# Optimization experiments

Measured on AMD Instinct MI355X. Metric: run time of the kernel, lower is better.

## Reference

```python
import jax, jax.numpy as jnp
import numpy as np

S, B, IN_DIM, HID, NT, TAPELEN = 256, 64, 128, 128, 2, 128
DIM = HID // NT          # per-tape cell width
LH = HID // 2            # LSTM hidden per direction


def _uniform(k, shape, fan):
    bound = 1.0 / np.sqrt(fan)
    return jax.random.uniform(k, shape, jnp.float32, -bound, bound)


def setup_inputs() -> dict:
    key = jax.random.key(0)
    ks = jax.random.split(key, 17)
    return {
        "inputs": jax.random.normal(ks[0], (S, B, IN_DIM), jnp.float32),
        "tapelen": TAPELEN,
        # bidirectional LSTM (torch gate order i,f,g,o)
        "W_ih_f": _uniform(ks[1], (4 * LH, IN_DIM), LH),
        "W_hh_f": _uniform(ks[2], (4 * LH, LH), LH),
        "b_ih_f": _uniform(ks[3], (4 * LH,), LH),
        "b_hh_f": _uniform(ks[4], (4 * LH,), LH),
        "W_ih_r": _uniform(ks[5], (4 * LH, IN_DIM), LH),
        "W_hh_r": _uniform(ks[6], (4 * LH, LH), LH),
        "b_ih_r": _uniform(ks[7], (4 * LH,), LH),
        "b_hh_r": _uniform(ks[8], (4 * LH,), LH),
        "W_act": _uniform(ks[9], (8 * NT, HID), HID),
        "b_act": _uniform(ks[10], (8 * NT,), HID),
        "W_val": _uniform(ks[11], (DIM * NT, IN_DIM), IN_DIM),
        "b_val": _uniform(ks[12], (DIM * NT,), IN_DIM),
        "W_out": _uniform(ks[13], (HID, HID), HID),
        "b_out": _uniform(ks[14], (HID,), HID),
    }


def _lstm_dir(x, Wih, Whh, bih, bhh, reverse):
    Hh = Whh.shape[1]
    bsz = x.shape[1]
    bias = bih + bhh

    def step(carry, xt):
        h, c = carry
        g = xt @ Wih.T + h @ Whh.T + bias
        i, f, gg, o = jnp.split(g, 4, axis=-1)
        c = jax.nn.sigmoid(f) * c + jax.nn.sigmoid(i) * jnp.tanh(gg)
        h = jax.nn.sigmoid(o) * jnp.tanh(c)
        return (h, c), h

    init = (jnp.zeros((bsz, Hh), x.dtype), jnp.zeros((bsz, Hh), x.dtype))
    _, hs = jax.lax.scan(step, init, x, reverse=reverse)
    return hs


def _nam_forward(inputs, tapelen, W_ih_f, W_hh_f, b_ih_f, b_hh_f,
                 W_ih_r, W_hh_r, b_ih_r, b_hh_r,
                 W_act, b_act, W_val, b_val, W_out, b_out):
    seqlen, bsz, _ = inputs.shape
    n_tapes = W_act.shape[0] // 8
    dim = W_val.shape[0] // n_tapes

    values = (inputs @ W_val.T + b_val).reshape(seqlen, bsz, n_tapes, dim)

    h_fwd = _lstm_dir(inputs, W_ih_f, W_hh_f, b_ih_f, b_hh_f, reverse=False)
    h_rev = _lstm_dir(inputs, W_ih_r, W_hh_r, b_ih_r, b_hh_r, reverse=True)
    hidden_control = jnp.concatenate([h_fwd, h_rev], axis=-1)  # [S,B,HID]

    actions = (hidden_control @ W_act.T + b_act).reshape(seqlen, bsz, n_tapes, 8)
    dir_r = jax.nn.softmax(actions[..., :3], axis=-1)
    dir_w = jax.nn.softmax(actions[..., 3:6], axis=-1)
    rwprobs = jax.nn.sigmoid(actions[..., 6:])

    tape0 = jnp.zeros((tapelen, bsz, n_tapes, dim), inputs.dtype)
    pos0 = jnp.zeros((tapelen, bsz, n_tapes), inputs.dtype).at[0].set(1.0)

    def step(carry, xs):
        tape, rpos, wpos = carry
        val, rdir, wdir, rw = xs  # [B,T,C], [B,T,3], [B,T,3], [B,T,2]
        oldval = jnp.einsum('lntc,lnt->ntc', tape, wpos)
        newmem = jnp.einsum('lnt,ntc->lntc', wpos, val - oldval)
        tape = tape + newmem * rw[None, :, :, 1:2]
        # NOTE: faithful to original — write-position shift uses rolls of rpos
        next_w = jnp.roll(rpos, 1, axis=0)
        prev_w = jnp.roll(rpos, -1, axis=0)
        wpos = (prev_w * wdir[None, :, :, 0] + wpos * wdir[None, :, :, 1]
                + next_w * wdir[None, :, :, 2])
        read_out = jnp.einsum('lntc,lnt->ntc', tape, rpos * rw[None, :, :, 0])
        next_r = jnp.roll(rpos, 1, axis=0)
        prev_r = jnp.roll(rpos, -1, axis=0)
        rpos = (prev_r * rdir[None, :, :, 0] + rpos * rdir[None, :, :, 1]
                + next_r * rdir[None, :, :, 2])
        return (tape, rpos, wpos), read_out

    (tape, rpos, wpos), read_outs = jax.lax.scan(
        step, (tape0, pos0, pos0), (values, dir_r, dir_w, rwprobs))

    outputs = read_outs.reshape(seqlen, bsz, -1) @ W_out.T + b_out
    return outputs, tape, rpos, wpos


def reference(inputs, tapelen, W_ih_f, W_hh_f, b_ih_f, b_hh_f,
              W_ih_r, W_hh_r, b_ih_r, b_hh_r,
              W_act, b_act, W_val, b_val, W_out, b_out):
    return _nam_forward(inputs, tapelen, W_ih_f, W_hh_f, b_ih_f, b_hh_f,
                        W_ih_r, W_hh_r, b_ih_r, b_hh_r,
                        W_act, b_act, W_val, b_val, W_out, b_out)
```

## Files before the change

### kernel.cpp

```cpp
#include <hip/hip_runtime.h>


typedef unsigned short u16;
typedef __attribute__((ext_vector_type(8))) __bf16 bf16x8;
typedef __attribute__((ext_vector_type(4))) float f32x4;

__device__ __forceinline__ u16 f2bf(float x) {
  unsigned u = __builtin_bit_cast(unsigned, x);
  u += 0x7fffu + ((u >> 16) & 1u);
  return (u16)(u >> 16);
}
__device__ __forceinline__ float sigm_f(float x) { return 1.f / (1.f + __expf(-x)); }
__device__ __forceinline__ float tanh_f(float x) { return 1.f - 2.f / (__expf(2.f * x) + 1.f); }

struct ConvArgs {
  const float* src[8];
  u16* dst[8];
  int off[9];
};

__global__ __launch_bounds__(256) void k_convert(ConvArgs a) {
  int total = a.off[8];
  for (int i = blockIdx.x * 256 + threadIdx.x; i < total; i += gridDim.x * 256) {
    int s = 0;
#pragma unroll
    for (int k = 1; k < 8; ++k) s += (i >= a.off[k]);
    int j = i - a.off[s];
    a.dst[s][j] = f2bf(a.src[s][j]);
  }
}

__device__ __forceinline__ void gemm_tile(const u16* A, const u16* W,
                                          const float* b1, const float* b2,
                                          float* C, int mt, int nt, int N, int lane) {
  const int rc = lane & 15;
  const int kq = lane >> 4;
  f32x4 acc = {0.f, 0.f, 0.f, 0.f};
#pragma unroll
  for (int kc = 0; kc < 4; ++kc) {
    bf16x8 av = *(const bf16x8*)(A + (size_t)(mt * 16 + rc) * 128 + kc * 32 + kq * 8);
    bf16x8 wv = *(const bf16x8*)(W + (size_t)(nt * 16 + rc) * 128 + kc * 32 + kq * 8);
    acc = __builtin_amdgcn_mfma_f32_16x16x32_bf16(av, wv, acc, 0, 0, 0);
  }
  const int n = nt * 16 + rc;
  float bias = b1[n] + (b2 ? b2[n] : 0.f);
  const int m0 = mt * 16 + kq * 4;
#pragma unroll
  for (int j = 0; j < 4; ++j) C[(size_t)(m0 + j) * N + n] = acc[j] + bias;
}

__global__ __launch_bounds__(256) void k_gemm_in(
    const u16* Abf, const u16* Wf, const u16* Wr, const u16* Wv,
    const float* bihf, const float* bhhf, const float* bihr, const float* bhhr,
    const float* bval, float* xf, float* xr, float* val) {
  int lane = threadIdx.x & 63;
  int wid = blockIdx.x * 4 + (threadIdx.x >> 6);
  if (wid < 16384) {
    gemm_tile(Abf, Wf, bihf, bhhf, xf, wid >> 4, wid & 15, 256, lane);
  } else if (wid < 32768) {
    int w2 = wid - 16384;
    gemm_tile(Abf, Wr, bihr, bhhr, xr, w2 >> 4, w2 & 15, 256, lane);
  } else {
    int w2 = wid - 32768;
    gemm_tile(Abf, Wv, bval, nullptr, val, w2 >> 3, w2 & 7, 128, lane);
  }
}

__global__ __launch_bounds__(256) void k_gemm_act(const u16* A, const u16* W,
                                                  const float* b1, float* C) {
  int lane = threadIdx.x & 63;
  int wid = blockIdx.x * 4 + (threadIdx.x >> 6);
  gemm_tile(A, W, b1, nullptr, C, wid, 0, 16, lane);
}

__global__ __launch_bounds__(256) void k_gemm_out(const u16* A, const u16* W,
                                                  const float* b1, float* C) {
  int lane = threadIdx.x & 63;
  int wid = blockIdx.x * 4 + (threadIdx.x >> 6);
  gemm_tile(A, W, b1, nullptr, C, wid >> 3, wid & 7, 128, lane);
}

__global__ __launch_bounds__(256) void k_lstm(
    const u16* Whhf, const u16* Whhr, const float* xpf, const float* xpr,
    u16* hidden_bf ) {
  const int tid = threadIdx.x;
  const int lane = tid & 63;
  const int v = __builtin_amdgcn_readfirstlane(tid >> 6);
  const int dir = blockIdx.x & 1;
  const int b_base = (blockIdx.x >> 1) * 16;
  const u16* Whh = dir ? Whhr : Whhf;
  const float* xp = dir ? xpr : xpf;

  __shared__ u16 h_lds[2][1024];
  for (int i = tid; i < 1024; i += 256) h_lds[0][i] = 0;

  const int cl = lane & 15;
  const int kq = lane >> 4;
  const int nbase = v * 16 + cl;
  const int rbase = b_base + kq * 4;

  bf16x8 wf[4][2];
#pragma unroll
  for (int gt = 0; gt < 4; ++gt)
#pragma unroll
    for (int kc = 0; kc < 2; ++kc)
      wf[gt][kc] = *(const bf16x8*)(Whh + (size_t)(gt * 64 + nbase) * 64 + kc * 32 + kq * 8);

  float c4[4] = {0.f, 0.f, 0.f, 0.f};
  float x0[16], x1[16];

#define LOADX(dst, ss)                                                       \
  _Pragma("unroll") for (int gt = 0; gt < 4; ++gt)                           \
  _Pragma("unroll") for (int j = 0; j < 4; ++j)                              \
    dst[gt * 4 + j] = xp[((size_t)(ss)*64 + rbase + j) * 256 + gt * 64 + nbase];

  { int s0 = dir ? 255 : 0; LOADX(x0, s0); }
  { int s1 = dir ? 254 : 1; LOADX(x1, s1); }

#define LSTM_STEP(XB, IT)                                                     \
  {                                                                           \
    const int it_ = (IT);                                                     \
    const int s_ = dir ? (255 - it_) : it_;                                   \
    __syncthreads();                                                          \
    bf16x8 af[2];                                                             \
    _Pragma("unroll") for (int kc = 0; kc < 2; ++kc) {                        \
      unsigned off = ((unsigned)(cl * 128 + kc * 64 + kq * 16)) ^             \
                     ((unsigned)(cl & 7) << 4);                               \
      af[kc] = *(const bf16x8*)((const char*)h_lds[it_ & 1] + off);           \
    }                                                                         \
    f32x4 acc[4];                                                             \
    _Pragma("unroll") for (int gt = 0; gt < 4; ++gt) {                        \
      f32x4 t_;                                                               \
      t_[0] = XB[gt * 4 + 0]; t_[1] = XB[gt * 4 + 1];                         \
      t_[2] = XB[gt * 4 + 2]; t_[3] = XB[gt * 4 + 3];                         \
      acc[gt] = t_;                                                           \
    }                                                                         \
    if (it_ + 2 < 256) { int sp_ = dir ? (253 - it_) : (it_ + 2); LOADX(XB, sp_); } \
    _Pragma("unroll") for (int kc = 0; kc < 2; ++kc)                          \
    _Pragma("unroll") for (int gt = 0; gt < 4; ++gt)                          \
      acc[gt] = __builtin_amdgcn_mfma_f32_16x16x32_bf16(af[kc], wf[gt][kc],   \
                                                        acc[gt], 0, 0, 0);    \
    u16* hw = h_lds[(it_ + 1) & 1];                                           \
    _Pragma("unroll") for (int j = 0; j < 4; ++j) {                           \
      float gi = sigm_f(acc[0][j]);                                           \
      float gf = sigm_f(acc[1][j]);                                           \
      float gg = tanh_f(acc[2][j]);                                           \
      float go = sigm_f(acc[3][j]);                                           \
      float cc = gf * c4[j] + gi * gg;                                        \
      c4[j] = cc;                                                             \
      float h_ = go * tanh_f(cc);                                             \
      u16 hv = f2bf(h_);                                                      \
      int row = kq * 4 + j;                                                   \
      unsigned off = ((unsigned)(row * 128 + nbase * 2)) ^                    \
                     ((unsigned)(row & 7) << 4);                              \
      *(u16*)((char*)hw + off) = hv;                                          \
      hidden_bf[((size_t)s_ * 64 + b_base + row) * 128 + dir * 64 + nbase] = hv; \
    }                                                                         \
  }

  for (int it2 = 0; it2 < 256; it2 += 2) {
    LSTM_STEP(x0, it2);
    LSTM_STEP(x1, it2 + 1);
  }
#undef LSTM_STEP
#undef LOADX
}

__global__ __launch_bounds__(256) void k_actsm(const float* raw, float* act) {
  int idx = blockIdx.x * 256 + threadIdx.x;
  const float* r = raw + (size_t)idx * 8;
  float4 d0 = *(const float4*)r;
  float4 d1 = *(const float4*)(r + 4);
  float m1 = fmaxf(fmaxf(d0.x, d0.y), d0.z);
  float e0 = __expf(d0.x - m1), e1 = __expf(d0.y - m1), e2 = __expf(d0.z - m1);
  float i1 = 1.f / (e0 + e1 + e2);
  float m2 = fmaxf(fmaxf(d0.w, d1.x), d1.y);
  float f0 = __expf(d0.w - m2), f1 = __expf(d1.x - m2), f2 = __expf(d1.y - m2);
  float i2 = 1.f / (f0 + f1 + f2);
  float rw0 = sigm_f(d1.z), rw1 = sigm_f(d1.w);
  float4* o = (float4*)(act + (size_t)idx * 8);
  o[0] = make_float4(e0 * i1, e1 * i1, e2 * i1, f0 * i2);
  o[1] = make_float4(f1 * i2, f2 * i2, rw0, rw1);
}

__global__ __launch_bounds__(64) void k_pos(const float* act, u16* wcoef, u16* rcoef,
                                            float* rw1arr, float* out_rpos, float* out_wpos) {
  const int bt = blockIdx.x;
  const int l = threadIdx.x;
  float rpe = (l == 0) ? 1.f : 0.f, rpo = 0.f;
  float wpe = rpe, wpo = 0.f;
  const float* abase = act + (size_t)bt * 8;
  float4 a0 = *(const float4*)abase;
  float4 a1 = *(const float4*)(abase + 4);
  unsigned* wcu = (unsigned*)wcoef;
  unsigned* rcu = (unsigned*)rcoef;
  for (int s = 0; s < 256; ++s) {
    float rd0 = a0.x, rd1 = a0.y, rd2 = a0.z;
    float wd0 = a0.w, wd1 = a1.x, wd2 = a1.y;
    float rw0 = a1.z, rw1 = a1.w;
    if (s + 1 < 256) {
      const float* an = abase + (size_t)(s + 1) * 1024;
      a0 = *(const float4*)an;
      a1 = *(const float4*)(an + 4);
    }
    size_t ci = ((size_t)s * 128 + bt) * 64 + l;
    wcu[ci] = (unsigned)f2bf(wpe) | ((unsigned)f2bf(wpo) << 16);
    rcu[ci] = (unsigned)f2bf(rpe * rw0) | ((unsigned)f2bf(rpo * rw0) << 16);
    if (l == 0) rw1arr[s * 128 + bt] = rw1;
    float up_odd = __shfl(rpo, (l + 63) & 63);
    float dn_even = __shfl(rpe, (l + 1) & 63);
    float n_e = up_odd, n_o = rpe;
    float p_e = rpo, p_o = dn_even;
    wpe = p_e * wd0 + wpe * wd1 + n_e * wd2;
    wpo = p_o * wd0 + wpo * wd1 + n_o * wd2;
    rpe = p_e * rd0 + rpe * rd1 + n_e * rd2;
    rpo = p_o * rd0 + rpo * rd1 + n_o * rd2;
  }
  int b = bt >> 1, tt = bt & 1;
  out_rpos[((size_t)(2 * l) * 64 + b) * 2 + tt] = rpe;
  out_rpos[((size_t)(2 * l + 1) * 64 + b) * 2 + tt] = rpo;
  out_wpos[((size_t)(2 * l) * 64 + b) * 2 + tt] = wpe;
  out_wpos[((size_t)(2 * l + 1) * 64 + b) * 2 + tt] = wpo;
}

__global__ __launch_bounds__(256) void k_tape(
    const float* values, const u16* wcoef, const u16* rcoef, const float* rw1arr,
    u16* readouts, float* out_tape) {
  const int bt = blockIdx.x;
  const int b = bt >> 1, t = bt & 1;
  const int tid = threadIdx.x;
  const int c = tid & 63;
  const int g = __builtin_amdgcn_readfirstlane(tid >> 6);
  __shared__ float lds_po[2][256];
  __shared__ float lds_pr[2][256];
  float tape[32];
#pragma unroll
  for (int j = 0; j < 32; ++j) tape[j] = 0.f;

  const unsigned* wcu = (const unsigned*)wcoef;
  const unsigned* rcu = (const unsigned*)rcoef;
  const size_t cbase = (size_t)bt * 64 + g * 16;
  const size_t vbase = (size_t)b * 128 + t * 64 + c;
  unsigned wA[16], rA[16], wB[16], rB[16];
  float rwA, rwB, vA, vB;
#pragma unroll
  for (int q = 0; q < 16; ++q) { wA[q] = wcu[cbase + q]; rA[q] = rcu[cbase + q]; }
  rwA = rw1arr[bt]; vA = values[vbase];
  {
    size_t nb = cbase + 8192;
#pragma unroll
    for (int q = 0; q < 16; ++q) { wB[q] = wcu[nb + q]; rB[q] = rcu[nb + q]; }
    rwB = rw1arr[128 + bt]; vB = values[8192 + vbase];
  }

#define TSTEP(CW, CR, CRW, CV, S)                                              \
  {                                                                            \
    const int s_ = (S);                                                        \
    float rwc = CRW, vcl = CV;                                                 \
    float wuf[32], ruf[32];                                                    \
    _Pragma("unroll") for (int q = 0; q < 16; ++q) {                           \
      wuf[2 * q] = __builtin_bit_cast(float, CW[q] << 16);                     \
      wuf[2 * q + 1] = __builtin_bit_cast(float, CW[q] & 0xffff0000u);         \
      ruf[2 * q] = __builtin_bit_cast(float, CR[q] << 16);                     \
      ruf[2 * q + 1] = __builtin_bit_cast(float, CR[q] & 0xffff0000u);         \
    }                                                                          \
    if (s_ + 2 < 256) {                                                        \
      size_t nb = cbase + (size_t)(s_ + 2) * 8192;                             \
      _Pragma("unroll") for (int q = 0; q < 16; ++q) {                         \
        CW[q] = wcu[nb + q]; CR[q] = rcu[nb + q]; }                            \
      CRW = rw1arr[(s_ + 2) * 128 + bt];                                       \
      CV = values[(size_t)(s_ + 2) * 8192 + vbase];                            \
    }                                                                          \
    float po = 0.f;                                                            \
    _Pragma("unroll") for (int j = 0; j < 32; ++j) po += tape[j] * wuf[j];     \
    lds_po[s_ & 1][(g << 6) + c] = po;                                         \
    __syncthreads();                                                           \
    if (g == 1 && s_ > 0) {                                                    \
      const float* pp = lds_pr[(s_ - 1) & 1];                                  \
      float ro = pp[c] + pp[64 + c] + pp[128 + c] + pp[192 + c];               \
      readouts[((size_t)(s_ - 1) * 64 + b) * 128 + t * 64 + c] = f2bf(ro);     \
    }                                                                          \
    const float* qq = lds_po[s_ & 1];                                          \
    float oldv = qq[c] + qq[64 + c] + qq[128 + c] + qq[192 + c];               \
    float dsc = rwc * (vcl - oldv);                                            \
    float pr = 0.f;                                                            \
    _Pragma("unroll") for (int j = 0; j < 32; ++j) {                           \
      tape[j] += wuf[j] * dsc;                                                 \
      pr += tape[j] * ruf[j];                                                  \
    }                                                                          \
    lds_pr[s_ & 1][(g << 6) + c] = pr;                                         \
  }

  for (int s = 0; s < 256; s += 2) {
    TSTEP(wA, rA, rwA, vA, s);
    TSTEP(wB, rB, rwB, vB, s + 1);
  }
#undef TSTEP
  __syncthreads();
  if (g == 1) {
    const float* pp = lds_pr[1];
    float ro = pp[c] + pp[64 + c] + pp[128 + c] + pp[192 + c];
    readouts[((size_t)255 * 64 + b) * 128 + t * 64 + c] = f2bf(ro);
  }
#pragma unroll
  for (int j = 0; j < 32; ++j) {
    int l = (g << 5) + j;
    out_tape[((size_t)(l * 64 + b) * 2 + t) * 64 + c] = tape[j];
  }
}

extern "C" void kernel_launch(void* const* d_in, const int* in_sizes, int n_in,
                              void* d_out, int out_size, void* d_ws, size_t ws_size,
                              hipStream_t stream) {
  const float* inputs = (const float*)d_in[0];
  const float* W_ih_f = (const float*)d_in[2];
  const float* W_hh_f = (const float*)d_in[3];
  const float* b_ih_f = (const float*)d_in[4];
  const float* b_hh_f = (const float*)d_in[5];
  const float* W_ih_r = (const float*)d_in[6];
  const float* W_hh_r = (const float*)d_in[7];
  const float* b_ih_r = (const float*)d_in[8];
  const float* b_hh_r = (const float*)d_in[9];
  const float* W_act  = (const float*)d_in[10];
  const float* b_act  = (const float*)d_in[11];
  const float* W_val  = (const float*)d_in[12];
  const float* b_val  = (const float*)d_in[13];
  const float* W_out  = (const float*)d_in[14];
  const float* b_out  = (const float*)d_in[15];

  char* ws = (char*)d_ws;
  u16* in_bf    = (u16*)(ws + 0);
  u16* wihf_bf  = (u16*)(ws + 4194304);
  u16* whhf_bf  = (u16*)(ws + 4259840);
  u16* wihr_bf  = (u16*)(ws + 4292608);
  u16* whhr_bf  = (u16*)(ws + 4358144);
  u16* wval_bf  = (u16*)(ws + 4390912);
  u16* wout_bf  = (u16*)(ws + 4423680);
  u16* wact_bf  = (u16*)(ws + 4456448);
  float* xf       = (float*)(ws + 4460544);
  float* xr       = (float*)(ws + 21237760);
  float* values   = (float*)(ws + 38014976);
  u16* hidden_bf  = (u16*)(ws + 46403584);
  float* actraw   = (float*)(ws + 50597888);
  float* act      = (float*)(ws + 52695040);
  u16* wcoef    = (u16*)(ws + 4460544);
  u16* rcoef    = (u16*)(ws + 12849152);
  float* rw1arr = (float*)(ws + 21237760);
  u16* readouts = (u16*)(ws + 21368832);

  float* out_outputs = (float*)d_out;
  float* out_tape = out_outputs + 2097152;
  float* out_rpos = out_outputs + 3145728;
  float* out_wpos = out_outputs + 3162112;

  ConvArgs ca;
  ca.src[0] = inputs; ca.dst[0] = in_bf;
  ca.src[1] = W_ih_f; ca.dst[1] = wihf_bf;
  ca.src[2] = W_hh_f; ca.dst[2] = whhf_bf;
  ca.src[3] = W_ih_r; ca.dst[3] = wihr_bf;
  ca.src[4] = W_hh_r; ca.dst[4] = whhr_bf;
  ca.src[5] = W_val;  ca.dst[5] = wval_bf;
  ca.src[6] = W_out;  ca.dst[6] = wout_bf;
  ca.src[7] = W_act;  ca.dst[7] = wact_bf;
  const int offs[9] = {0, 2097152, 2129920, 2146304, 2179072, 2195456,
                       2211840, 2228224, 2230272};
  for (int i = 0; i < 9; ++i) ca.off[i] = offs[i];

  hipLaunchKernelGGL(k_convert, dim3(4352), dim3(256), 0, stream, ca);
  hipLaunchKernelGGL(k_gemm_in, dim3(10240), dim3(256), 0, stream,
                     in_bf, wihf_bf, wihr_bf, wval_bf,
                     b_ih_f, b_hh_f, b_ih_r, b_hh_r, b_val, xf, xr, values);
  hipLaunchKernelGGL(k_lstm, dim3(8), dim3(256), 0, stream,
                     whhf_bf, whhr_bf, xf, xr, hidden_bf);
  hipLaunchKernelGGL(k_gemm_act, dim3(512), dim3(256), 0, stream,
                     hidden_bf, wact_bf, b_act, actraw);
  hipLaunchKernelGGL(k_actsm, dim3(128), dim3(256), 0, stream, actraw, act);
  hipLaunchKernelGGL(k_pos, dim3(128), dim3(64), 0, stream,
                     act, wcoef, rcoef, rw1arr, out_rpos, out_wpos);
  hipLaunchKernelGGL(k_tape, dim3(128), dim3(256), 0, stream,
                     values, wcoef, rcoef, rw1arr, readouts, out_tape);
  hipLaunchKernelGGL(k_gemm_out, dim3(2048), dim3(256), 0, stream,
                     readouts, wout_bf, b_out, out_outputs);
}
```

Before: 655.3 us.

## Restructure LSTM input layout, fuse activation softmax into pos kernel, add tape2

```diff
diff --git a/kernel.cpp b/kernel.cpp
--- a/kernel.cpp
+++ b/kernel.cpp
@@ -20,19 +20,26 @@
 };
 
 __global__ __launch_bounds__(256) void k_convert(ConvArgs a) {
-  int total = a.off[8];
-  for (int i = blockIdx.x * 256 + threadIdx.x; i < total; i += gridDim.x * 256) {
-    int s = 0;
-#pragma unroll
-    for (int k = 1; k < 8; ++k) s += (i >= a.off[k]);
-    int j = i - a.off[s];
+  int i = blockIdx.x * 256 + threadIdx.x;
+  if (i < 524288) {
+    float4 vv = ((const float4*)a.src[0])[i];
+    uint2 o;
+    o.x = (unsigned)f2bf(vv.x) | ((unsigned)f2bf(vv.y) << 16);
+    o.y = (unsigned)f2bf(vv.z) | ((unsigned)f2bf(vv.w) << 16);
+    ((uint2*)a.dst[0])[i] = o;
+  } else if (i < 657408) {
+    int ii = i - 524288 + 2097152;
+    int s = 1;
+#pragma unroll
+    for (int k = 2; k < 8; ++k) s += (ii >= a.off[k]);
+    int j = ii - a.off[s];
     a.dst[s][j] = f2bf(a.src[s][j]);
   }
 }
 
 __device__ __forceinline__ void gemm_tile(const u16* A, const u16* W,
-                                          const float* b1, const float* b2,
-                                          float* C, int mt, int nt, int N, int lane) {
+                                          const float* b1, float* C,
+                                          int mt, int nt, int N, int lane) {
   const int rc = lane & 15;
   const int kq = lane >> 4;
   f32x4 acc = {0.f, 0.f, 0.f, 0.f};
@@ -43,51 +50,81 @@
     acc = __builtin_amdgcn_mfma_f32_16x16x32_bf16(av, wv, acc, 0, 0, 0);
   }
   const int n = nt * 16 + rc;
-  float bias = b1[n] + (b2 ? b2[n] : 0.f);
+  float bias = b1[n];
   const int m0 = mt * 16 + kq * 4;
 #pragma unroll
   for (int j = 0; j < 4; ++j) C[(size_t)(m0 + j) * N + n] = acc[j] + bias;
 }
 
+__device__ __forceinline__ void gemm_tile_xp(const u16* A, const u16* W,
+                                             const float* b1, const float* b2,
+                                             float* X, int mt, int nt, int lane) {
+  const int rc = lane & 15;
+  const int kq = lane >> 4;
+  f32x4 acc = {0.f, 0.f, 0.f, 0.f};
+#pragma unroll
+  for (int kc = 0; kc < 4; ++kc) {
+    bf16x8 av = *(const bf16x8*)(A + (size_t)(mt * 16 + rc) * 128 + kc * 32 + kq * 8);
+    bf16x8 wv = *(const bf16x8*)(W + (size_t)(nt * 16 + rc) * 128 + kc * 32 + kq * 8);
+    acc = __builtin_amdgcn_mfma_f32_16x16x32_bf16(av, wv, acc, 0, 0, 0);
+  }
+  const int n = nt * 16 + rc;
+  const float bias = b1[n] + b2[n];
+  const int m0 = mt * 16 + kq * 4;
+  const int s = m0 >> 6, brow0 = m0 & 63;
+  const int cb = brow0 >> 4, kq2 = (brow0 & 15) >> 2;
+  const int gt = n >> 6, v2 = (n >> 4) & 3, cl2 = n & 15;
+  unsigned off = (((unsigned)(s * 4 + cb) * 4 + kq2) * 64 + v2 * 16 + cl2) * 16 + gt * 4;
+  f32x4 o;
+#pragma unroll
+  for (int j = 0; j < 4; ++j) o[j] = acc[j] + bias;
+  *(f32x4*)(X + off) = o;
+}
+
 __global__ __launch_bounds__(256) void k_gemm_in(
-    const u16* Abf, const u16* Wf, const u16* Wr, const u16* Wv,
+    const u16* __restrict__ Abf, const u16* __restrict__ Wf,
+    const u16* __restrict__ Wr, const u16* __restrict__ Wv,
     const float* bihf, const float* bhhf, const float* bihr, const float* bhhr,
     const float* bval, float* xf, float* xr, float* val) {
   int lane = threadIdx.x & 63;
   int wid = blockIdx.x * 4 + (threadIdx.x >> 6);
   if (wid < 16384) {
-    gemm_tile(Abf, Wf, bihf, bhhf, xf, wid >> 4, wid & 15, 256, lane);
+    gemm_tile_xp(Abf, Wf, bihf, bhhf, xf, wid >> 4, wid & 15, lane);
   } else if (wid < 32768) {
     int w2 = wid - 16384;
-    gemm_tile(Abf, Wr, bihr, bhhr, xr, w2 >> 4, w2 & 15, 256, lane);
+    gemm_tile_xp(Abf, Wr, bihr, bhhr, xr, w2 >> 4, w2 & 15, lane);
   } else {
     int w2 = wid - 32768;
-    gemm_tile(Abf, Wv, bval, nullptr, val, w2 >> 3, w2 & 7, 128, lane);
-  }
-}
-
-__global__ __launch_bounds__(256) void k_gemm_act(const u16* A, const u16* W,
+    gemm_tile(Abf, Wv, bval, val, w2 >> 3, w2 & 7, 128, lane);
+  }
+}
+
+__global__ __launch_bounds__(256) void k_gemm_act(const u16* __restrict__ A,
+                                                  const u16* __restrict__ W,
                                                   const float* b1, float* C) {
   int lane = threadIdx.x & 63;
   int wid = blockIdx.x * 4 + (threadIdx.x >> 6);
-  gemm_tile(A, W, b1, nullptr, C, wid, 0, 16, lane);
-}
-
-__global__ __launch_bounds__(256) void k_gemm_out(const u16* A, const u16* W,
+  gemm_tile(A, W, b1, C, wid, 0, 16, lane);
+}
+
+__global__ __launch_bounds__(256) void k_gemm_out(const u16* __restrict__ A,
+                                                  const u16* __restrict__ W,
                                                   const float* b1, float* C) {
   int lane = threadIdx.x & 63;
   int wid = blockIdx.x * 4 + (threadIdx.x >> 6);
-  gemm_tile(A, W, b1, nullptr, C, wid >> 3, wid & 7, 128, lane);
-}
-
-__global__ __launch_bounds__(256) void k_lstm(
-    const u16* Whhf, const u16* Whhr, const float* xpf, const float* xpr,
-    u16* hidden_bf ) {
+  gemm_tile(A, W, b1, C, wid >> 3, wid & 7, 128, lane);
+}
+
+__global__ __launch_bounds__(256, 1) void k_lstm(
+    const u16* __restrict__ Whhf, const u16* __restrict__ Whhr,
+    const float* __restrict__ xpf, const float* __restrict__ xpr,
+    u16* __restrict__ hidden_bf ) {
   const int tid = threadIdx.x;
   const int lane = tid & 63;
   const int v = __builtin_amdgcn_readfirstlane(tid >> 6);
   const int dir = blockIdx.x & 1;
-  const int b_base = (blockIdx.x >> 1) * 16;
+  const int cb = blockIdx.x >> 1;
+  const int b_base = cb * 16;
   const u16* Whh = dir ? Whhr : Whhf;
   const float* xp = dir ? xpr : xpf;
 
@@ -97,7 +134,6 @@
   const int cl = lane & 15;
   const int kq = lane >> 4;
   const int nbase = v * 16 + cl;
-  const int rbase = b_base + kq * 4;
 
   bf16x8 wf[4][2];
 #pragma unroll
@@ -107,101 +143,121 @@
       wf[gt][kc] = *(const bf16x8*)(Whh + (size_t)(gt * 64 + nbase) * 64 + kc * 32 + kq * 8);
 
   float c4[4] = {0.f, 0.f, 0.f, 0.f};
-  float x0[16], x1[16];
-
-#define LOADX(dst, ss)                                                       \
-  _Pragma("unroll") for (int gt = 0; gt < 4; ++gt)                           \
-  _Pragma("unroll") for (int j = 0; j < 4; ++j)                              \
-    dst[gt * 4 + j] = xp[((size_t)(ss)*64 + rbase + j) * 256 + gt * 64 + nbase];
-
-  { int s0 = dir ? 255 : 0; LOADX(x0, s0); }
-  { int s1 = dir ? 254 : 1; LOADX(x1, s1); }
-
-#define LSTM_STEP(XB, IT)                                                     \
-  {                                                                           \
-    const int it_ = (IT);                                                     \
-    const int s_ = dir ? (255 - it_) : it_;                                   \
-    __syncthreads();                                                          \
-    bf16x8 af[2];                                                             \
-    _Pragma("unroll") for (int kc = 0; kc < 2; ++kc) {                        \
-      unsigned off = ((unsigned)(cl * 128 + kc * 64 + kq * 16)) ^             \
-                     ((unsigned)(cl & 7) << 4);                               \
-      af[kc] = *(const bf16x8*)((const char*)h_lds[it_ & 1] + off);           \
-    }                                                                         \
-    f32x4 acc[4];                                                             \
-    _Pragma("unroll") for (int gt = 0; gt < 4; ++gt) {                        \
-      f32x4 t_;                                                               \
-      t_[0] = XB[gt * 4 + 0]; t_[1] = XB[gt * 4 + 1];                         \
-      t_[2] = XB[gt * 4 + 2]; t_[3] = XB[gt * 4 + 3];                         \
-      acc[gt] = t_;                                                           \
-    }                                                                         \
-    if (it_ + 2 < 256) { int sp_ = dir ? (253 - it_) : (it_ + 2); LOADX(XB, sp_); } \
-    _Pragma("unroll") for (int kc = 0; kc < 2; ++kc)                          \
-    _Pragma("unroll") for (int gt = 0; gt < 4; ++gt)                          \
-      acc[gt] = __builtin_amdgcn_mfma_f32_16x16x32_bf16(af[kc], wf[gt][kc],   \
-                                                        acc[gt], 0, 0, 0);    \
-    u16* hw = h_lds[(it_ + 1) & 1];                                           \
-    _Pragma("unroll") for (int j = 0; j < 4; ++j) {                           \
-      float gi = sigm_f(acc[0][j]);                                           \
-      float gf = sigm_f(acc[1][j]);                                           \
-      float gg = tanh_f(acc[2][j]);                                           \
-      float go = sigm_f(acc[3][j]);                                           \
-      float cc = gf * c4[j] + gi * gg;                                        \
-      c4[j] = cc;                                                             \
-      float h_ = go * tanh_f(cc);                                             \
-      u16 hv = f2bf(h_);                                                      \
-      int row = kq * 4 + j;                                                   \
-      unsigned off = ((unsigned)(row * 128 + nbase * 2)) ^                    \
-                     ((unsigned)(row & 7) << 4);                              \
-      *(u16*)((char*)hw + off) = hv;                                          \
-      hidden_bf[((size_t)s_ * 64 + b_base + row) * 128 + dir * 64 + nbase] = hv; \
-    }                                                                         \
+
+  const unsigned tconst = (unsigned)kq * 1024u + (unsigned)nbase * 16u;
+  const int s0i = dir ? 255 : 0, s1i = dir ? 254 : 1;
+  unsigned x0off = (unsigned)(s0i * 4 + cb) * 4096u + tconst;
+  unsigned x1off = (unsigned)(s1i * 4 + cb) * 4096u + tconst;
+  const unsigned xstride = dir ? (unsigned)(-32768) : 32768u;
+
+  const unsigned dsrc = ((unsigned)tid * 8u) ^ ((((unsigned)tid >> 4) & 7u) << 4);
+  unsigned hoff = (unsigned)(dir ? 255 : 0) * 16384u +
+                  (unsigned)(b_base + (tid >> 4)) * 256u + (unsigned)dir * 128u +
+                  ((unsigned)tid & 15u) * 8u;
+  const unsigned hstride = dir ? (unsigned)(-16384) : 16384u;
+
+  unsigned aw[4];
+#pragma unroll
+  for (int j = 0; j < 4; ++j) {
+    unsigned r = (unsigned)(kq * 4 + j);
+    aw[j] = (r * 128u + (unsigned)nbase * 2u) ^ ((r & 7u) << 4);
+  }
+  unsigned ar[2];
+#pragma unroll
+  for (int kc = 0; kc < 2; ++kc)
+    ar[kc] = ((unsigned)(cl * 128 + kc * 64 + kq * 16)) ^ (((unsigned)cl & 7u) << 4);
+
+  f32x4 x0[4], x1[4];
+#define LOADX(X, OFF)                                                          \
+  {                                                                            \
+    const f32x4* p_ = (const f32x4*)(xp + OFF);                                \
+    X[0] = p_[0]; X[1] = p_[1]; X[2] = p_[2]; X[3] = p_[3];                    \
+  }
+  LOADX(x0, x0off);
+  LOADX(x1, x1off);
+  x0off += xstride; x1off += xstride;
+
+#define LSTM_STEP(XB, XOFF, IT, PAR)                                           \
+  {                                                                            \
+    const int it_ = (IT);                                                      \
+    __syncthreads();                                                           \
+    if (it_ > 0) {                           \
+      uint2 hv2 = *(const uint2*)((const char*)h_lds + ((PAR) << 11) + dsrc);  \
+      *(uint2*)((char*)hidden_bf + hoff) = hv2;                                \
+      hoff += hstride;                                                         \
+    }                                                                          \
+    bf16x8 af[2];                                                              \
+    _Pragma("unroll") for (int kc = 0; kc < 2; ++kc)                           \
+      af[kc] = *(const bf16x8*)((const char*)h_lds + ((PAR) << 11) + ar[kc]);  \
+    f32x4 acc[4];                                                              \
+    _Pragma("unroll") for (int gt = 0; gt < 4; ++gt)                           \
+      acc[gt] = __builtin_amdgcn_mfma_f32_16x16x32_bf16(af[0], wf[gt][0],      \
+                                                        XB[gt], 0, 0, 0);      \
+    if (it_ + 2 < 256) { LOADX(XB, XOFF); XOFF += xstride; }                   \
+    _Pragma("unroll") for (int gt = 0; gt < 4; ++gt)                           \
+      acc[gt] = __builtin_amdgcn_mfma_f32_16x16x32_bf16(af[1], wf[gt][1],      \
+                                                        acc[gt], 0, 0, 0);     \
+    float hh[4];                                                               \
+    _Pragma("unroll") for (int j = 0; j < 4; ++j) {                            \
+      float gi = sigm_f(acc[0][j]);                                            \
+      float gf = sigm_f(acc[1][j]);                                            \
+      float gg = tanh_f(acc[2][j]);                                            \
+      float go = sigm_f(acc[3][j]);                                            \
+      float cc = gf * c4[j] + gi * gg;                                         \
+      c4[j] = cc;                                                              \
+      hh[j] = go * tanh_f(cc);                                                 \
+    }                                                                          \
+    unsigned p01, p23;                                                         \
+    asm("v_cvt_pk_bf16_f32 %0, %1, %2" : "=v"(p01) : "v"(hh[0]), "v"(hh[1]));  \
+    asm("v_cvt_pk_bf16_f32 %0, %1, %2" : "=v"(p23) : "v"(hh[2]), "v"(hh[3]));  \
+    char* hw = (char*)h_lds + ((1 - (PAR)) << 11);                             \
+    *(u16*)(hw + aw[0]) = (u16)p01;                                            \
+    *(u16*)(hw + aw[1]) = (u16)(p01 >> 16);                                    \
+    *(u16*)(hw + aw[2]) = (u16)p23;                                            \
+    *(u16*)(hw + aw[3]) = (u16)(p23 >> 16);                                    \
   }
 
   for (int it2 = 0; it2 < 256; it2 += 2) {
-    LSTM_STEP(x0, it2);
-    LSTM_STEP(x1, it2 + 1);
+    LSTM_STEP(x0, x0off, it2, 0);
+    LSTM_STEP(x1, x1off, it2 + 1, 1);
   }
 #undef LSTM_STEP
 #undef LOADX
-}
-
-__global__ __launch_bounds__(256) void k_actsm(const float* raw, float* act) {
-  int idx = blockIdx.x * 256 + threadIdx.x;
-  const float* r = raw + (size_t)idx * 8;
-  float4 d0 = *(const float4*)r;
-  float4 d1 = *(const float4*)(r + 4);
-  float m1 = fmaxf(fmaxf(d0.x, d0.y), d0.z);
-  float e0 = __expf(d0.x - m1), e1 = __expf(d0.y - m1), e2 = __expf(d0.z - m1);
-  float i1 = 1.f / (e0 + e1 + e2);
-  float m2 = fmaxf(fmaxf(d0.w, d1.x), d1.y);
-  float f0 = __expf(d0.w - m2), f1 = __expf(d1.x - m2), f2 = __expf(d1.y - m2);
-  float i2 = 1.f / (f0 + f1 + f2);
-  float rw0 = sigm_f(d1.z), rw1 = sigm_f(d1.w);
-  float4* o = (float4*)(act + (size_t)idx * 8);
-  o[0] = make_float4(e0 * i1, e1 * i1, e2 * i1, f0 * i2);
-  o[1] = make_float4(f1 * i2, f2 * i2, rw0, rw1);
-}
-
-__global__ __launch_bounds__(64) void k_pos(const float* act, u16* wcoef, u16* rcoef,
+
+  __syncthreads();
+  {
+    uint2 hv2 = *(const uint2*)((const char*)h_lds + dsrc);
+    *(uint2*)((char*)hidden_bf + hoff) = hv2;
+  }
+}
+
+__global__ __launch_bounds__(64) void k_pos(const float* __restrict__ raw,
+                                            u16* __restrict__ wcoef, u16* __restrict__ rcoef,
                                             float* rw1arr, float* out_rpos, float* out_wpos) {
   const int bt = blockIdx.x;
   const int l = threadIdx.x;
+  const int b = bt >> 1, tt = bt & 1;
+  const float* abase = raw + (size_t)b * 16 + tt * 8;
+  float4 d0 = *(const float4*)abase;
+  float4 d1 = *(const float4*)(abase + 4);
   float rpe = (l == 0) ? 1.f : 0.f, rpo = 0.f;
   float wpe = rpe, wpo = 0.f;
-  const float* abase = act + (size_t)bt * 8;
-  float4 a0 = *(const float4*)abase;
-  float4 a1 = *(const float4*)(abase + 4);
   unsigned* wcu = (unsigned*)wcoef;
   unsigned* rcu = (unsigned*)rcoef;
   for (int s = 0; s < 256; ++s) {
-    float rd0 = a0.x, rd1 = a0.y, rd2 = a0.z;
-    float wd0 = a0.w, wd1 = a1.x, wd2 = a1.y;
-    float rw0 = a1.z, rw1 = a1.w;
+    float m1 = fmaxf(fmaxf(d0.x, d0.y), d0.z);
+    float e0 = __expf(d0.x - m1), e1 = __expf(d0.y - m1), e2 = __expf(d0.z - m1);
+    float i1 = 1.f / (e0 + e1 + e2);
+    float m2 = fmaxf(fmaxf(d0.w, d1.x), d1.y);
+    float f0 = __expf(d0.w - m2), f1 = __expf(d1.x - m2), f2 = __expf(d1.y - m2);
+    float i2 = 1.f / (f0 + f1 + f2);
+    float rd0 = e0 * i1, rd1 = e1 * i1, rd2 = e2 * i1;
+    float wd0 = f0 * i2, wd1 = f1 * i2, wd2 = f2 * i2;
+    float rw0 = sigm_f(d1.z), rw1 = sigm_f(d1.w);
     if (s + 1 < 256) {
       const float* an = abase + (size_t)(s + 1) * 1024;
-      a0 = *(const float4*)an;
-      a1 = *(const float4*)(an + 4);
+      d0 = *(const float4*)an;
+      d1 = *(const float4*)(an + 4);
     }
     size_t ci = ((size_t)s * 128 + bt) * 64 + l;
     wcu[ci] = (unsigned)f2bf(wpe) | ((unsigned)f2bf(wpo) << 16);
@@ -216,16 +272,16 @@
     rpe = p_e * rd0 + rpe * rd1 + n_e * rd2;
     rpo = p_o * rd0 + rpo * rd1 + n_o * rd2;
   }
-  int b = bt >> 1, tt = bt & 1;
   out_rpos[((size_t)(2 * l) * 64 + b) * 2 + tt] = rpe;
   out_rpos[((size_t)(2 * l + 1) * 64 + b) * 2 + tt] = rpo;
   out_wpos[((size_t)(2 * l) * 64 + b) * 2 + tt] = wpe;
   out_wpos[((size_t)(2 * l + 1) * 64 + b) * 2 + tt] = wpo;
 }
 
-__global__ __launch_bounds__(256) void k_tape(
-    const float* values, const u16* wcoef, const u16* rcoef, const float* rw1arr,
-    u16* readouts, float* out_tape) {
+__global__ __launch_bounds__(256, 1) void k_tape(
+    const float* __restrict__ values, const u16* __restrict__ wcoef,
+    const u16* __restrict__ rcoef, const float* __restrict__ rw1arr,
+    u16* __restrict__ readouts, float* __restrict__ out_tape) {
   const int bt = blockIdx.x;
   const int b = bt >> 1, t = bt & 1;
   const int tid = threadIdx.x;
@@ -253,16 +309,16 @@
     rwB = rw1arr[128 + bt]; vB = values[8192 + vbase];
   }
 
+#define BCF(u) __builtin_bit_cast(float, (u))
 #define TSTEP(CW, CR, CRW, CV, S)                                              \
   {                                                                            \
     const int s_ = (S);                                                        \
     float rwc = CRW, vcl = CV;                                                 \
-    float wuf[32], ruf[32];                                                    \
+    float po_[4] = {0.f, 0.f, 0.f, 0.f};                                       \
     _Pragma("unroll") for (int q = 0; q < 16; ++q) {                           \
-      wuf[2 * q] = __builtin_bit_cast(float, CW[q] << 16);                     \
-      wuf[2 * q + 1] = __builtin_bit_cast(float, CW[q] & 0xffff0000u);         \
-      ruf[2 * q] = __builtin_bit_cast(float, CR[q] << 16);                     \
-      ruf[2 * q + 1] = __builtin_bit_cast(float, CR[q] & 0xffff0000u);         \
+      unsigned cw = (unsigned)__builtin_amdgcn_readfirstlane(CW[q]);           \
+      po_[q & 3] += tape[2 * q] * BCF(cw << 16);                               \
+      po_[q & 3] += tape[2 * q + 1] * BCF(cw & 0xffff0000u);                   \
     }                                                                          \
     if (s_ + 2 < 256) {                                                        \
       size_t nb = cbase + (size_t)(s_ + 2) * 8192;                             \
@@ -271,24 +327,26 @@
       CRW = rw1arr[(s_ + 2) * 128 + bt];                                       \
       CV = values[(size_t)(s_ + 2) * 8192 + vbase];                            \
     }                                                                          \
-    float po = 0.f;                                                            \
-    _Pragma("unroll") for (int j = 0; j < 32; ++j) po += tape[j] * wuf[j];     \
-    lds_po[s_ & 1][(g << 6) + c] = po;                                         \
+    lds_po[s_ & 1][(g << 6) + c] = (po_[0] + po_[1]) + (po_[2] + po_[3]);      \
     __syncthreads();                                                           \
     if (g == 1 && s_ > 0) {                                                    \
       const float* pp = lds_pr[(s_ - 1) & 1];                                  \
-      float ro = pp[c] + pp[64 + c] + pp[128 + c] + pp[192 + c];               \
+      float ro = (pp[c] + pp[64 + c]) + (pp[128 + c] + pp[192 + c]);           \
       readouts[((size_t)(s_ - 1) * 64 + b) * 128 + t * 64 + c] = f2bf(ro);     \
     }                                                                          \
     const float* qq = lds_po[s_ & 1];                                          \
-    float oldv = qq[c] + qq[64 + c] + qq[128 + c] + qq[192 + c];               \
+    float oldv = (qq[c] + qq[64 + c]) + (qq[128 + c] + qq[192 + c]);           \
     float dsc = rwc * (vcl - oldv);                                            \
-    float pr = 0.f;                                                            \
-    _Pragma("unroll") for (int j = 0; j < 32; ++j) {                           \
-      tape[j] += wuf[j] * dsc;                                                 \
-      pr += tape[j] * ruf[j];                                                  \
-    }                                                                          \
-    lds_pr[s_ & 1][(g << 6) + c] = pr;                                         \
+    float pr_[4] = {0.f, 0.f, 0.f, 0.f};                                       \
+    _Pragma("unroll") for (int q = 0; q < 16; ++q) {                           \
+      unsigned cw = (unsigned)__builtin_amdgcn_readfirstlane(CW[q]);           \
+      unsigned cr = (unsigned)__builtin_amdgcn_readfirstlane(CR[q]);           \
+      tape[2 * q] += BCF(cw << 16) * dsc;                                      \
+      pr_[q & 3] += tape[2 * q] * BCF(cr << 16);                               \
+      tape[2 * q + 1] += BCF(cw & 0xffff0000u) * dsc;                          \
+      pr_[q & 3] += tape[2 * q + 1] * BCF(cr & 0xffff0000u);                   \
+    }                                                                          \
+    lds_pr[s_ & 1][(g << 6) + c] = (pr_[0] + pr_[1]) + (pr_[2] + pr_[3]);      \
   }
 
   for (int s = 0; s < 256; s += 2) {
@@ -296,10 +354,102 @@
     TSTEP(wB, rB, rwB, vB, s + 1);
   }
 #undef TSTEP
+#undef BCF
   __syncthreads();
   if (g == 1) {
     const float* pp = lds_pr[1];
-    float ro = pp[c] + pp[64 + c] + pp[128 + c] + pp[192 + c];
+    float ro = (pp[c] + pp[64 + c]) + (pp[128 + c] + pp[192 + c]);
+    readouts[((size_t)255 * 64 + b) * 128 + t * 64 + c] = f2bf(ro);
+  }
+#pragma unroll
+  for (int j = 0; j < 32; ++j) {
+    int l = (g << 5) + j;
+    out_tape[((size_t)(l * 64 + b) * 2 + t) * 64 + c] = tape[j];
+  }
+}
+
+
+__global__ __launch_bounds__(256, 1) void k_tape2(
+    const float* __restrict__ values, const u16* __restrict__ wcoef,
+    const u16* __restrict__ rcoef, const float* __restrict__ rw1arr,
+    u16* __restrict__ readouts, float* __restrict__ out_tape) {
+  const int bt = blockIdx.x;
+  const int b = bt >> 1, t = bt & 1;
+  const int tid = threadIdx.x;
+  const int c = tid & 63;
+  const int g = __builtin_amdgcn_readfirstlane(tid >> 6);
+  __shared__ float lds_po[2][256];
+  __shared__ float lds_pr[2][256];
+  float tape[32];
+#pragma unroll
+  for (int j = 0; j < 32; ++j) tape[j] = 0.f;
+
+  const unsigned* wcu = (const unsigned*)wcoef;
+  const unsigned* rcu = (const unsigned*)rcoef;
+  const size_t cbase = (size_t)bt * 64 + g * 16;
+  const size_t vbase = (size_t)b * 128 + t * 64 + c;
+  unsigned wA[16], rA[16], wB[16], rB[16];
+  float rwA, rwB, vA, vB;
+#pragma unroll
+  for (int q = 0; q < 16; ++q) { wA[q] = wcu[cbase + q]; rA[q] = rcu[cbase + q]; }
+  rwA = rw1arr[bt]; vA = values[vbase];
+  {
+    size_t nb = cbase + 8192;
+#pragma unroll
+    for (int q = 0; q < 16; ++q) { wB[q] = wcu[nb + q]; rB[q] = rcu[nb + q]; }
+    rwB = rw1arr[128 + bt]; vB = values[8192 + vbase];
+  }
+
+#define BCF(u) __builtin_bit_cast(float, (u))
+#define TSTEP(CW, CR, CRW, CV, S)                                              \
+  {                                                                            \
+    const int s_ = (S);                                                        \
+    float rwc = CRW, vcl = CV;                                                 \
+    float wsc[32], rsc[32];                                                    \
+    _Pragma("unroll") for (int q = 0; q < 16; ++q) {                           \
+      unsigned cw = (unsigned)__builtin_amdgcn_readfirstlane(CW[q]);           \
+      unsigned cr = (unsigned)__builtin_amdgcn_readfirstlane(CR[q]);           \
+      wsc[2 * q] = BCF(cw << 16);  wsc[2 * q + 1] = BCF(cw & 0xffff0000u);     \
+      rsc[2 * q] = BCF(cr << 16);  rsc[2 * q + 1] = BCF(cr & 0xffff0000u);     \
+    }                                                                          \
+    float po_[4] = {0.f, 0.f, 0.f, 0.f};                                       \
+    _Pragma("unroll") for (int j = 0; j < 32; ++j)                             \
+      po_[j & 3] += tape[j] * wsc[j];                                          \
+    if (s_ + 2 < 256) {                                                        \
+      size_t nb = cbase + (size_t)(s_ + 2) * 8192;                             \
+      _Pragma("unroll") for (int q = 0; q < 16; ++q) {                         \
+        CW[q] = wcu[nb + q]; CR[q] = rcu[nb + q]; }                            \
+      CRW = rw1arr[(s_ + 2) * 128 + bt];                                       \
+      CV = values[(size_t)(s_ + 2) * 8192 + vbase];                            \
+    }                                                                          \
+    lds_po[s_ & 1][(g << 6) + c] = (po_[0] + po_[1]) + (po_[2] + po_[3]);      \
+    __syncthreads();                                                           \
+    if (g == 1 && s_ > 0) {                                                    \
+      const float* pp = lds_pr[(s_ - 1) & 1];                                  \
+      float ro = (pp[c] + pp[64 + c]) + (pp[128 + c] + pp[192 + c]);           \
+      readouts[((size_t)(s_ - 1) * 64 + b) * 128 + t * 64 + c] = f2bf(ro);     \
+    }                                                                          \
+    const float* qq = lds_po[s_ & 1];                                          \
+    float oldv = (qq[c] + qq[64 + c]) + (qq[128 + c] + qq[192 + c]);           \
+    float dsc = rwc * (vcl - oldv);                                            \
+    float pr_[4] = {0.f, 0.f, 0.f, 0.f};                                       \
+    _Pragma("unroll") for (int j = 0; j < 32; ++j) {                           \
+      tape[j] += wsc[j] * dsc;                                                 \
+      pr_[j & 3] += tape[j] * rsc[j];                                          \
+    }                                                                          \
+    lds_pr[s_ & 1][(g << 6) + c] = (pr_[0] + pr_[1]) + (pr_[2] + pr_[3]);      \
+  }
+
+  for (int s = 0; s < 256; s += 2) {
+    TSTEP(wA, rA, rwA, vA, s);
+    TSTEP(wB, rB, rwB, vB, s + 1);
+  }
+#undef TSTEP
+#undef BCF
+  __syncthreads();
+  if (g == 1) {
+    const float* pp = lds_pr[1];
+    float ro = (pp[c] + pp[64 + c]) + (pp[128 + c] + pp[192 + c]);
     readouts[((size_t)255 * 64 + b) * 128 + t * 64 + c] = f2bf(ro);
   }
 #pragma unroll
@@ -342,7 +492,6 @@
   float* values   = (float*)(ws + 38014976);
   u16* hidden_bf  = (u16*)(ws + 46403584);
   float* actraw   = (float*)(ws + 50597888);
-  float* act      = (float*)(ws + 52695040);
   u16* wcoef    = (u16*)(ws + 4460544);
   u16* rcoef    = (u16*)(ws + 12849152);
   float* rw1arr = (float*)(ws + 21237760);
@@ -366,7 +515,7 @@
                        2211840, 2228224, 2230272};
   for (int i = 0; i < 9; ++i) ca.off[i] = offs[i];
 
-  hipLaunchKernelGGL(k_convert, dim3(4352), dim3(256), 0, stream, ca);
+  hipLaunchKernelGGL(k_convert, dim3(2568), dim3(256), 0, stream, ca);
   hipLaunchKernelGGL(k_gemm_in, dim3(10240), dim3(256), 0, stream,
                      in_bf, wihf_bf, wihr_bf, wval_bf,
                      b_ih_f, b_hh_f, b_ih_r, b_hh_r, b_val, xf, xr, values);
@@ -374,10 +523,9 @@
                      whhf_bf, whhr_bf, xf, xr, hidden_bf);
   hipLaunchKernelGGL(k_gemm_act, dim3(512), dim3(256), 0, stream,
                      hidden_bf, wact_bf, b_act, actraw);
-  hipLaunchKernelGGL(k_actsm, dim3(128), dim3(256), 0, stream, actraw, act);
   hipLaunchKernelGGL(k_pos, dim3(128), dim3(64), 0, stream,
-                     act, wcoef, rcoef, rw1arr, out_rpos, out_wpos);
-  hipLaunchKernelGGL(k_tape, dim3(128), dim3(256), 0, stream,
+                     actraw, wcoef, rcoef, rw1arr, out_rpos, out_wpos);
+  hipLaunchKernelGGL(k_tape2, dim3(128), dim3(256), 0, stream,
                      values, wcoef, rcoef, rw1arr, readouts, out_tape);
   hipLaunchKernelGGL(k_gemm_out, dim3(2048), dim3(256), 0, stream,
                      readouts, wout_bf, b_out, out_outputs);
```

After: 678.1 us. 1.03x slower.
